# Kernel tuning notes

Measured on AMD Instinct MI355X. Metric: run time of the kernel, lower is better.

## Reference

```python
import jax, jax.numpy as jnp
import numpy as np

N_NODES = 100000

def _sage_layer(x, src, dst, W_self, W_neigh, b, act):
    # DGL SAGEConv 'mean': h = fc_self(x) + fc_neigh(mean_{u->v} x_u) + bias
    msg_sum = jax.ops.segment_sum(x[src], dst, num_segments=N_NODES)  # [N, d]
    deg = jax.ops.segment_sum(jnp.ones((src.shape[0], 1), x.dtype), dst, num_segments=N_NODES)
    h_neigh = msg_sum / jnp.maximum(deg, 1.0)
    h = x @ W_self + h_neigh @ W_neigh + b
    return jax.nn.relu(h) if act else h

def _edge_score(h, s, d, W1, b1, W2, b2):
    e = jnp.concatenate([h[s], h[d]], axis=-1)  # [E, 2*64]
    return (jax.nn.relu(e @ W1 + b1) @ W2 + b2).squeeze(-1)  # [E]

def setup_inputs() -> dict:
    key = jax.random.key(0)
    ks = jax.random.split(key, 16)
    E, EP = 1000000, 200000
    d_in, d_hid, d_out = 512, 256, 64
    def lin(k, fan_in, shape):
        return jax.random.normal(k, shape, dtype=jnp.float32) * (1.0 / np.sqrt(fan_in))
    return {
        "x": jax.random.normal(ks[0], (N_NODES, d_in), dtype=jnp.float32),
        "src": jax.random.randint(ks[1], (E,), 0, N_NODES, dtype=jnp.int32),
        "dst": jax.random.randint(ks[2], (E,), 0, N_NODES, dtype=jnp.int32),
        "pos_src": jax.random.randint(ks[3], (EP,), 0, N_NODES, dtype=jnp.int32),
        "pos_dst": jax.random.randint(ks[4], (EP,), 0, N_NODES, dtype=jnp.int32),
        "neg_src": jax.random.randint(ks[5], (EP,), 0, N_NODES, dtype=jnp.int32),
        "neg_dst": jax.random.randint(ks[6], (EP,), 0, N_NODES, dtype=jnp.int32),
        "W_self1": lin(ks[7], d_in, (d_in, d_hid)),
        "W_neigh1": lin(ks[8], d_in, (d_in, d_hid)),
        "b1": jnp.zeros((d_hid,), jnp.float32),
        "W_self2": lin(ks[9], d_hid, (d_hid, d_out)),
        "W_neigh2": lin(ks[10], d_hid, (d_hid, d_out)),
        "b2": jnp.zeros((d_out,), jnp.float32),
        "Wp1": lin(ks[11], 2 * d_out, (2 * d_out, d_out)),
        "bp1": jnp.zeros((d_out,), jnp.float32),
        "Wp2": lin(ks[12], d_out, (d_out, 1)),
        "bp2": jnp.zeros((1,), jnp.float32),
    }

def reference(x, src, dst, pos_src, pos_dst, neg_src, neg_dst,
              W_self1, W_neigh1, b1, W_self2, W_neigh2, b2,
              Wp1, bp1, Wp2, bp2):
    h = _sage_layer(x, src, dst, W_self1, W_neigh1, b1, act=True)
    h = _sage_layer(h, src, dst, W_self2, W_neigh2, b2, act=False)
    pos_score = _edge_score(h, pos_src, pos_dst, Wp1, bp1, Wp2, bp2)
    neg_score = _edge_score(h, neg_src, neg_dst, Wp1, bp1, Wp2, bp2)
    return (pos_score, neg_score)
```

## Files before the change

### kernel.cpp

```cpp
#include <hip/hip_runtime.h>
#include <hip/hip_bf16.h>


#define N_NODES 100000
#define N_EDGES 1000000
#define EPOS    200000
#define NSB     391

typedef unsigned short u16;
typedef unsigned int   u32;

typedef __bf16 bf16x8 __attribute__((ext_vector_type(8)));
typedef float  f32x4  __attribute__((ext_vector_type(4)));
typedef u16    u16x8  __attribute__((ext_vector_type(8)));

__device__ __forceinline__ u16 f2bf(float f) {
  u32 u = __float_as_uint(f);
  u32 r = (u + 0x7fffu + ((u >> 16) & 1u)) >> 16;
  return (u16)r;
}
__device__ __forceinline__ float bf2f(u16 h) {
  return __uint_as_float(((u32)h) << 16);
}

__device__ __forceinline__ void gl_lds16(const void* g, void* l) {
  __builtin_amdgcn_global_load_lds(
      (const __attribute__((address_space(1))) void*)g,
      (__attribute__((address_space(3))) void*)l, 16, 0, 0);
}

__global__ __launch_bounds__(256) void k_prep(
    const float* __restrict__ x, u16* __restrict__ xb,
    const int* __restrict__ dst, int* __restrict__ deg, int* __restrict__ epos,
    const float* __restrict__ Ws1, const float* __restrict__ Wn1, u16* __restrict__ W1t,
    const float* __restrict__ Ws2, const float* __restrict__ Wn2, u16* __restrict__ W2t,
    const float* __restrict__ Wp1, u16* __restrict__ Wpt) {
  const int bid = blockIdx.x;
  const int tid = threadIdx.x;
  if (bid < 25000) {
    long i = ((long)bid * 256 + tid) * 8;
    float4 f0 = *(const float4*)(x + i);
    float4 f1 = *(const float4*)(x + i + 4);
    u16x8 o;
    o[0] = f2bf(f0.x); o[1] = f2bf(f0.y); o[2] = f2bf(f0.z); o[3] = f2bf(f0.w);
    o[4] = f2bf(f1.x); o[5] = f2bf(f1.y); o[6] = f2bf(f1.z); o[7] = f2bf(f1.w);
    *(u16x8*)(xb + i) = o;
  } else if (bid < 28907) {
    int e = (bid - 25000) * 256 + tid;
    if (e < N_EDGES) epos[e] = atomicAdd(&deg[dst[e]], 1);
  } else if (bid < 29931) {
    int idx = (bid - 28907) * 256 + tid;
    int j = idx >> 9, k = idx & 511;
    float v = (j < 256) ? Ws1[k * 256 + j] : Wn1[k * 256 + (j - 256)];
    W1t[idx] = f2bf(v);
  } else if (bid < 30059) {
    int idx = (bid - 29931) * 256 + tid;
    int j = idx >> 8, k = idx & 255;
    float v = (j < 64) ? Ws2[k * 64 + j] : Wn2[k * 64 + (j - 64)];
    W2t[idx] = f2bf(v);
  } else {
    int idx = (bid - 30059) * 256 + tid;
    int j = idx >> 6, k = idx & 63;
    float v = (j < 64) ? Wp1[k * 64 + j] : Wp1[(64 + k) * 64 + (j - 64)];
    Wpt[idx] = f2bf(v);
  }
}

__global__ __launch_bounds__(256) void k_scan_a(const int* __restrict__ deg,
                                                int* __restrict__ bsum) {
  __shared__ int s[256];
  int i = blockIdx.x * 256 + threadIdx.x;
  s[threadIdx.x] = (i < N_NODES) ? deg[i] : 0;
  __syncthreads();
  for (int off = 128; off > 0; off >>= 1) {
    if (threadIdx.x < off) s[threadIdx.x] += s[threadIdx.x + off];
    __syncthreads();
  }
  if (threadIdx.x == 0) bsum[blockIdx.x] = s[0];
}

__global__ __launch_bounds__(512) void k_scan_b(int* __restrict__ bsum) {
  __shared__ int s[512];
  const int t = threadIdx.x;
  int v = (t < NSB) ? bsum[t] : 0;
  s[t] = v;
  __syncthreads();
  for (int off = 1; off < 512; off <<= 1) {
    int w = (t >= off) ? s[t - off] : 0;
    __syncthreads();
    s[t] += w;
    __syncthreads();
  }
  if (t < NSB) bsum[t] = s[t] - v;
}

__global__ __launch_bounds__(256) void k_scan_c(const int* __restrict__ deg,
                                                const int* __restrict__ bsum,
                                                int* __restrict__ offs,
                                                float* __restrict__ invdeg) {
  __shared__ int s[256];
  const int t = threadIdx.x;
  const int i = blockIdx.x * 256 + t;
  const int d = (i < N_NODES) ? deg[i] : 0;
  s[t] = d;
  __syncthreads();
  for (int off = 1; off < 256; off <<= 1) {
    int w = (t >= off) ? s[t - off] : 0;
    __syncthreads();
    s[t] += w;
    __syncthreads();
  }
  if (i < N_NODES) {
    const int base = bsum[blockIdx.x];
    offs[i] = base + s[t] - d;
    invdeg[i] = 1.0f / (float)(d > 0 ? d : 1);
    if (i == N_NODES - 1) offs[N_NODES] = base + s[t];
  }
}

__global__ void k_fill(const int* __restrict__ src, const int* __restrict__ dst,
                       const int* __restrict__ offs, const int* __restrict__ epos,
                       int* __restrict__ csr) {
  int i = blockIdx.x * 256 + threadIdx.x;
  if (i < N_EDGES) csr[offs[dst[i]] + epos[i]] = src[i];
}

template <bool OUT_F32, bool SWZ1>
__global__ __launch_bounds__(256) void gemm_bt(const u16* __restrict__ A,
                                               const u16* __restrict__ Bt,
                                               void* __restrict__ Cv,
                                               int M, int N, int K) {
  __shared__ u16 As[2][4096];
  __shared__ u16 Bs[2][4096];
  const int tid  = threadIdx.x;
  const int lane = tid & 63;
  const int wid  = tid >> 6;
  const int wr   = wid >> 1, wc = wid & 1;
  int bm0, bn0;
  if (SWZ1) {
    const int d = blockIdx.x;
    const int s = (d & 7) * 391 + (d >> 3);
    bm0 = (s >> 2) * 128;
    bn0 = (s & 3) * 128;
  } else {
    bm0 = blockIdx.y * 128;
    bn0 = blockIdx.x * 128;
  }

  const int sr = tid >> 2;
  const int sc = (tid & 3) * 8;
  const u16* pa0 = A  + (long)min(bm0 + sr,      M - 1) * K + sc;
  const u16* pa1 = A  + (long)min(bm0 + sr + 64, M - 1) * K + sc;
  const u16* pb0 = Bt + (long)(bn0 + sr)      * K + sc;
  const u16* pb1 = Bt + (long)(bn0 + sr + 64) * K + sc;
  const int lw = wid * 512;

  f32x4 acc[4][4];
#pragma unroll
  for (int i = 0; i < 4; ++i)
#pragma unroll
    for (int j = 0; j < 4; ++j) {
      f32x4 z = {0.f, 0.f, 0.f, 0.f};
      acc[i][j] = z;
    }

  const int nk = K >> 5;
#define STAGE(buf, kk) do { const int k0_ = (kk) << 5;                    \
    gl_lds16(pa0 + k0_, &As[buf][lw]);                                    \
    gl_lds16(pa1 + k0_, &As[buf][2048 + lw]);                             \
    gl_lds16(pb0 + k0_, &Bs[buf][lw]);                                    \
    gl_lds16(pb1 + k0_, &Bs[buf][2048 + lw]); } while (0)

  STAGE(0, 0);
  __syncthreads();
  int cur = 0;
  for (int kk = 0; kk < nk; ++kk) {
    if (kk + 1 < nk) STAGE(cur ^ 1, kk + 1);
    bf16x8 af[4], bfr[4];
#pragma unroll
    for (int mi = 0; mi < 4; ++mi)
      af[mi] = *reinterpret_cast<const bf16x8*>(
          &As[cur][(wr * 64 + mi * 16 + (lane & 15)) * 32 + ((lane >> 4) * 8)]);
#pragma unroll
    for (int ni = 0; ni < 4; ++ni)
      bfr[ni] = *reinterpret_cast<const bf16x8*>(
          &Bs[cur][(wc * 64 + ni * 16 + (lane & 15)) * 32 + ((lane >> 4) * 8)]);
#pragma unroll
    for (int mi = 0; mi < 4; ++mi)
#pragma unroll
      for (int ni = 0; ni < 4; ++ni)
        acc[mi][ni] = __builtin_amdgcn_mfma_f32_16x16x32_bf16(
            af[mi], bfr[ni], acc[mi][ni], 0, 0, 0);
    __syncthreads();
    cur ^= 1;
  }
#undef STAGE

  const int colb = bn0 + wc * 64 + (lane & 15);
  const int rowb = bm0 + wr * 64 + ((lane >> 4) * 4);
#pragma unroll
  for (int mi = 0; mi < 4; ++mi) {
#pragma unroll
    for (int ni = 0; ni < 4; ++ni) {
      const int col = colb + ni * 16;
#pragma unroll
      for (int e = 0; e < 4; ++e) {
        const int row = rowb + mi * 16 + e;
        if (row < M) {
          if (OUT_F32)
            ((float*)Cv)[(long)row * N + col] = acc[mi][ni][e];
          else
            ((u16*)Cv)[(long)row * N + col] = f2bf(acc[mi][ni][e]);
        }
      }
    }
  }
}

__global__ __launch_bounds__(256) void k_agg1(const u16* __restrict__ z1b,
                                              const int* __restrict__ csr,
                                              const int* __restrict__ offs,
                                              const float* __restrict__ invdeg,
                                              const float* __restrict__ b1,
                                              u16* __restrict__ h1b) {
  const int v    = blockIdx.x * 4 + (threadIdx.x >> 6);
  const int lane = threadIdx.x & 63;
  const int c    = lane * 4;
  const int o0 = offs[v], o1 = offs[v + 1];
  float a0 = 0.f, a1 = 0.f, a2 = 0.f, a3 = 0.f;
  int i = o0;
  for (; i + 8 <= o1; i += 8) {
    ushort4 q[8];
#pragma unroll
    for (int t = 0; t < 8; ++t)
      q[t] = *(const ushort4*)&z1b[(long)csr[i + t] * 512 + 256 + c];
#pragma unroll
    for (int t = 0; t < 8; ++t) {
      a0 += bf2f(q[t].x); a1 += bf2f(q[t].y);
      a2 += bf2f(q[t].z); a3 += bf2f(q[t].w);
    }
  }
  if (i + 4 <= o1) {
    ushort4 q[4];
#pragma unroll
    for (int t = 0; t < 4; ++t)
      q[t] = *(const ushort4*)&z1b[(long)csr[i + t] * 512 + 256 + c];
#pragma unroll
    for (int t = 0; t < 4; ++t) {
      a0 += bf2f(q[t].x); a1 += bf2f(q[t].y);
      a2 += bf2f(q[t].z); a3 += bf2f(q[t].w);
    }
    i += 4;
  }
  for (; i < o1; ++i) {
    ushort4 q = *(const ushort4*)&z1b[(long)csr[i] * 512 + 256 + c];
    a0 += bf2f(q.x); a1 += bf2f(q.y); a2 += bf2f(q.z); a3 += bf2f(q.w);
  }
  const float w = invdeg[v];
  ushort4 sf = *(const ushort4*)&z1b[(long)v * 512 + c];
  float4 bb = *(const float4*)&b1[c];
  ushort4 o;
  o.x = f2bf(fmaxf(bf2f(sf.x) + a0 * w + bb.x, 0.f));
  o.y = f2bf(fmaxf(bf2f(sf.y) + a1 * w + bb.y, 0.f));
  o.z = f2bf(fmaxf(bf2f(sf.z) + a2 * w + bb.z, 0.f));
  o.w = f2bf(fmaxf(bf2f(sf.w) + a3 * w + bb.w, 0.f));
  *(ushort4*)&h1b[(long)v * 256 + c] = o;
}

__global__ __launch_bounds__(256) void k_agg2(const u16* __restrict__ z2b,
                                              const int* __restrict__ csr,
                                              const int* __restrict__ offs,
                                              const float* __restrict__ invdeg,
                                              const float* __restrict__ b2,
                                              u16* __restrict__ h2b) {
  const int v    = blockIdx.x * 4 + (threadIdx.x >> 6);
  const int lane = threadIdx.x & 63;
  const int half = lane >> 5;
  const int c    = (lane & 31) * 2;
  const int o0 = offs[v], o1 = offs[v + 1];
  float a0 = 0.f, a1 = 0.f;
  int i = o0 + half;
  for (; i + 6 < o1; i += 8) {
    u32 q0 = *(const u32*)&z2b[(long)csr[i]     * 128 + 64 + c];
    u32 q1 = *(const u32*)&z2b[(long)csr[i + 2] * 128 + 64 + c];
    u32 q2 = *(const u32*)&z2b[(long)csr[i + 4] * 128 + 64 + c];
    u32 q3 = *(const u32*)&z2b[(long)csr[i + 6] * 128 + 64 + c];
    a0 += (bf2f((u16)q0) + bf2f((u16)q1)) + (bf2f((u16)q2) + bf2f((u16)q3));
    a1 += (bf2f((u16)(q0 >> 16)) + bf2f((u16)(q1 >> 16))) +
          (bf2f((u16)(q2 >> 16)) + bf2f((u16)(q3 >> 16)));
  }
  for (; i < o1; i += 2) {
    const u32 q = *(const u32*)&z2b[(long)csr[i] * 128 + 64 + c];
    a0 += bf2f((u16)q);
    a1 += bf2f((u16)(q >> 16));
  }
  a0 += __shfl_xor(a0, 32);
  a1 += __shfl_xor(a1, 32);
  if (half == 0) {
    const float w = invdeg[v];
    const u32 sq = *(const u32*)&z2b[(long)v * 128 + c];
    float h0 = bf2f((u16)sq) + a0 * w + b2[c];
    float h1 = bf2f((u16)(sq >> 16)) + a1 * w + b2[c + 1];
    u32 o = (u32)f2bf(h0) | ((u32)f2bf(h1) << 16);
    *(u32*)&h2b[(long)v * 64 + c] = o;
  }
}

__global__ __launch_bounds__(256) void k_edge(const u16* __restrict__ UVb,
                                              const int* __restrict__ ps,
                                              const int* __restrict__ pd,
                                              const int* __restrict__ ns,
                                              const int* __restrict__ nd,
                                              const float* __restrict__ bp1,
                                              const float* __restrict__ Wp2,
                                              const float* __restrict__ bp2,
                                              float* __restrict__ out) {
  const int g    = blockIdx.x * 4 + (threadIdx.x >> 6);
  const int lane = threadIdx.x & 63;
  const int half = lane >> 5;
  const int l    = lane & 31;
  int s, d;
  if (g < EPOS) { s = ps[g]; d = pd[g]; }
  else          { s = ns[g - EPOS]; d = nd[g - EPOS]; }
  const int node = half ? d : s;
  const u32 q = *(const u32*)&UVb[(long)node * 128 + half * 64 + 2 * l];
  float t0 = bf2f((u16)q), t1 = bf2f((u16)(q >> 16));
  t0 += __shfl_xor(t0, 32);
  t1 += __shfl_xor(t1, 32);
  const float2 bb = *(const float2*)&bp1[2 * l];
  const float2 ww = *(const float2*)&Wp2[2 * l];
  float p = fmaxf(t0 + bb.x, 0.f) * ww.x + fmaxf(t1 + bb.y, 0.f) * ww.y;
#pragma unroll
  for (int off = 16; off > 0; off >>= 1) p += __shfl_xor(p, off);
  if (lane == 0) out[g] = p + bp2[0];
}

extern "C" void kernel_launch(void* const* d_in, const int* in_sizes, int n_in,
                              void* d_out, int out_size, void* d_ws, size_t ws_size,
                              hipStream_t stream) {
  const float* x   = (const float*)d_in[0];
  const int*   src = (const int*)d_in[1];
  const int*   dst = (const int*)d_in[2];
  const int*   ps  = (const int*)d_in[3];
  const int*   pd  = (const int*)d_in[4];
  const int*   ns  = (const int*)d_in[5];
  const int*   nd  = (const int*)d_in[6];
  const float* Ws1 = (const float*)d_in[7];
  const float* Wn1 = (const float*)d_in[8];
  const float* b1  = (const float*)d_in[9];
  const float* Ws2 = (const float*)d_in[10];
  const float* Wn2 = (const float*)d_in[11];
  const float* b2  = (const float*)d_in[12];
  const float* Wp1 = (const float*)d_in[13];
  const float* bp1 = (const float*)d_in[14];
  const float* Wp2 = (const float*)d_in[15];
  const float* bp2 = (const float*)d_in[16];
  float* out = (float*)d_out;

  char* ws = (char*)d_ws;
  const size_t RB = 102400000;
  const size_t RC = 204800000;
  u16*   xb  = (u16*)(ws);
  u16*   h1b = (u16*)(ws);
  u16*   UVb = (u16*)(ws + 51200000);
  int*   epos= (int*)(ws + RB);
  u16*   z1b = (u16*)(ws + RB);
  u16*   z2b = (u16*)(ws + RB);
  u16*   h2b = (u16*)(ws + RB + 25600000);
  size_t o = RC;
  u16*   W1t = (u16*)(ws + o); o += 524288;
  u16*   W2t = (u16*)(ws + o); o += 65536;
  u16*   Wpt = (u16*)(ws + o); o += 16384;
  int*   deg = (int*)(ws + o); o += 400128;
  int*   offs= (int*)(ws + o); o += 400128;
  float* idg = (float*)(ws + o); o += 400128;
  int*   bsum= (int*)(ws + o); o += 2048;
  int*   csr = (int*)(ws + o); o += 4000000;
  (void)ws_size; (void)in_sizes; (void)n_in; (void)out_size;

  hipMemsetAsync(deg, 0, 400128, stream);

  k_prep<<<30091, 256, 0, stream>>>(x, xb, dst, deg, epos,
                                    Ws1, Wn1, W1t, Ws2, Wn2, W2t, Wp1, Wpt);
  k_scan_a<<<NSB, 256, 0, stream>>>(deg, bsum);
  k_scan_b<<<1, 512, 0, stream>>>(bsum);
  k_scan_c<<<NSB, 256, 0, stream>>>(deg, bsum, offs, idg);
  k_fill<<<3907, 256, 0, stream>>>(src, dst, offs, epos, csr);

  gemm_bt<false, true><<<3128, 256, 0, stream>>>(xb, W1t, z1b, N_NODES, 512, 512);
  k_agg1<<<25000, 256, 0, stream>>>(z1b, csr, offs, idg, b1, h1b);
  gemm_bt<false, false><<<dim3(1, 782), 256, 0, stream>>>(h1b, W2t, z2b, N_NODES, 128, 256);
  k_agg2<<<25000, 256, 0, stream>>>(z2b, csr, offs, idg, b2, h2b);
  gemm_bt<false, false><<<dim3(1, 782), 256, 0, stream>>>(h2b, Wpt, UVb, N_NODES, 128, 64);
  k_edge<<<100000, 256, 0, stream>>>(UVb, ps, pd, ns, nd, bp1, Wp2, bp2, out);
}
```

Baseline: 716.0 us.

## Fuse fp32-to-bf16 conversion of x into first GEMM and widen agg1 loads

Drops the separate pass that converted x to bf16 inside k_prep. The first GEMM now reads fp32 x directly, converts in registers, and writes to LDS, saving a 100 MB write and 100 MB re-read of xb. Because there are 4 column tiles, the first GEMM now reads the fp32 A rows from global memory once per column tile. Separately, k_agg1 now uses 16-byte loads with two half-waves splitting each node's edges and combining partial sums via a shuffle.

```diff
diff --git a/kernel.cpp b/kernel.cpp
--- a/kernel.cpp
+++ b/kernel.cpp
@@ -22,6 +22,12 @@
 __device__ __forceinline__ float bf2f(u16 h) {
   return __uint_as_float(((u32)h) << 16);
 }
+__device__ __forceinline__ u16x8 cvt8(float4 lo, float4 hi) {
+  u16x8 o;
+  o[0] = f2bf(lo.x); o[1] = f2bf(lo.y); o[2] = f2bf(lo.z); o[3] = f2bf(lo.w);
+  o[4] = f2bf(hi.x); o[5] = f2bf(hi.y); o[6] = f2bf(hi.z); o[7] = f2bf(hi.w);
+  return o;
+}
 
 __device__ __forceinline__ void gl_lds16(const void* g, void* l) {
   __builtin_amdgcn_global_load_lds(
@@ -30,36 +36,27 @@
 }
 
 __global__ __launch_bounds__(256) void k_prep(
-    const float* __restrict__ x, u16* __restrict__ xb,
     const int* __restrict__ dst, int* __restrict__ deg, int* __restrict__ epos,
     const float* __restrict__ Ws1, const float* __restrict__ Wn1, u16* __restrict__ W1t,
     const float* __restrict__ Ws2, const float* __restrict__ Wn2, u16* __restrict__ W2t,
     const float* __restrict__ Wp1, u16* __restrict__ Wpt) {
   const int bid = blockIdx.x;
   const int tid = threadIdx.x;
-  if (bid < 25000) {
-    long i = ((long)bid * 256 + tid) * 8;
-    float4 f0 = *(const float4*)(x + i);
-    float4 f1 = *(const float4*)(x + i + 4);
-    u16x8 o;
-    o[0] = f2bf(f0.x); o[1] = f2bf(f0.y); o[2] = f2bf(f0.z); o[3] = f2bf(f0.w);
-    o[4] = f2bf(f1.x); o[5] = f2bf(f1.y); o[6] = f2bf(f1.z); o[7] = f2bf(f1.w);
-    *(u16x8*)(xb + i) = o;
-  } else if (bid < 28907) {
-    int e = (bid - 25000) * 256 + tid;
+  if (bid < 3907) {
+    int e = bid * 256 + tid;
     if (e < N_EDGES) epos[e] = atomicAdd(&deg[dst[e]], 1);
-  } else if (bid < 29931) {
-    int idx = (bid - 28907) * 256 + tid;
+  } else if (bid < 4931) {
+    int idx = (bid - 3907) * 256 + tid;
     int j = idx >> 9, k = idx & 511;
     float v = (j < 256) ? Ws1[k * 256 + j] : Wn1[k * 256 + (j - 256)];
     W1t[idx] = f2bf(v);
-  } else if (bid < 30059) {
-    int idx = (bid - 29931) * 256 + tid;
+  } else if (bid < 5059) {
+    int idx = (bid - 4931) * 256 + tid;
     int j = idx >> 8, k = idx & 255;
     float v = (j < 64) ? Ws2[k * 64 + j] : Wn2[k * 64 + (j - 64)];
     W2t[idx] = f2bf(v);
   } else {
-    int idx = (bid - 30059) * 256 + tid;
+    int idx = (bid - 5059) * 256 + tid;
     int j = idx >> 6, k = idx & 63;
     float v = (j < 64) ? Wp1[k * 64 + j] : Wp1[(64 + k) * 64 + (j - 64)];
     Wpt[idx] = f2bf(v);
@@ -125,10 +122,96 @@
   if (i < N_EDGES) csr[offs[dst[i]] + epos[i]] = src[i];
 }
 
-template <bool OUT_F32, bool SWZ1>
+__global__ __launch_bounds__(256) void gemm1_f32(const float* __restrict__ A,
+                                                 const u16* __restrict__ Bt,
+                                                 u16* __restrict__ C, int M) {
+  const int K = 512, N = 512;
+  __shared__ u16 As[2][4096];
+  __shared__ u16 Bs[2][4096];
+  const int tid  = threadIdx.x;
+  const int lane = tid & 63;
+  const int wid  = tid >> 6;
+  const int wr   = wid >> 1, wc = wid & 1;
+  const int d    = blockIdx.x;
+  const int s    = (d & 7) * 391 + (d >> 3);
+  const int bm0  = (s >> 2) * 128;
+  const int bn0  = (s & 3) * 128;
+
+  const int sr = tid >> 2;
+  const int sc = (tid & 3) * 8;
+  const float* pa0 = A + (long)min(bm0 + sr,      M - 1) * K + sc;
+  const float* pa1 = A + (long)min(bm0 + sr + 64, M - 1) * K + sc;
+  const u16*   pb0 = Bt + (long)(bn0 + sr)      * K + sc;
+  const u16*   pb1 = Bt + (long)(bn0 + sr + 64) * K + sc;
+  const int lw = wid * 512;
+
+  f32x4 acc[4][4];
+#pragma unroll
+  for (int i = 0; i < 4; ++i)
+#pragma unroll
+    for (int j = 0; j < 4; ++j) {
+      f32x4 z = {0.f, 0.f, 0.f, 0.f};
+      acc[i][j] = z;
+    }
+
+  float4 r00, r01, r10, r11;
+#define LOADA(kk) do { const int k0_ = (kk) << 5;                         \
+    r00 = *(const float4*)(pa0 + k0_); r01 = *(const float4*)(pa0 + k0_ + 4); \
+    r10 = *(const float4*)(pa1 + k0_); r11 = *(const float4*)(pa1 + k0_ + 4); } while (0)
+#define STAGEB(buf, kk) do { const int k0_ = (kk) << 5;                   \
+    gl_lds16(pb0 + k0_, &Bs[buf][lw]);                                    \
+    gl_lds16(pb1 + k0_, &Bs[buf][2048 + lw]); } while (0)
+#define CVW(buf) do {                                                     \
+    *(u16x8*)&As[buf][sr * 32 + sc]        = cvt8(r00, r01);              \
+    *(u16x8*)&As[buf][(sr + 64) * 32 + sc] = cvt8(r10, r11); } while (0)
+
+  LOADA(0); STAGEB(0, 0); CVW(0);
+  __syncthreads();
+  int cur = 0;
+  const int nk = K >> 5;
+  for (int kk = 0; kk < nk; ++kk) {
+    if (kk + 1 < nk) { LOADA(kk + 1); STAGEB(cur ^ 1, kk + 1); }
+    bf16x8 af[4], bfr[4];
+#pragma unroll
+    for (int mi = 0; mi < 4; ++mi)
+      af[mi] = *reinterpret_cast<const bf16x8*>(
+          &As[cur][(wr * 64 + mi * 16 + (lane & 15)) * 32 + ((lane >> 4) * 8)]);
+#pragma unroll
+    for (int ni = 0; ni < 4; ++ni)
+      bfr[ni] = *reinterpret_cast<const bf16x8*>(
+          &Bs[cur][(wc * 64 + ni * 16 + (lane & 15)) * 32 + ((lane >> 4) * 8)]);
+#pragma unroll
+    for (int mi = 0; mi < 4; ++mi)
+#pragma unroll
+      for (int ni = 0; ni < 4; ++ni)
+        acc[mi][ni] = __builtin_amdgcn_mfma_f32_16x16x32_bf16(
+            af[mi], bfr[ni], acc[mi][ni], 0, 0, 0);
+    if (kk + 1 < nk) CVW(cur ^ 1);
+    __syncthreads();
+    cur ^= 1;
+  }
+#undef LOADA
+#undef STAGEB
+#undef CVW
+
+  const int colb = bn0 + wc * 64 + (lane & 15);
+  const int rowb = bm0 + wr * 64 + ((lane >> 4) * 4);
+#pragma unroll
+  for (int mi = 0; mi < 4; ++mi)
+#pragma unroll
+    for (int ni = 0; ni < 4; ++ni) {
+      const int col = colb + ni * 16;
+#pragma unroll
+      for (int e = 0; e < 4; ++e) {
+        const int row = rowb + mi * 16 + e;
+        if (row < M) C[(long)row * N + col] = f2bf(acc[mi][ni][e]);
+      }
+    }
+}
+
 __global__ __launch_bounds__(256) void gemm_bt(const u16* __restrict__ A,
                                                const u16* __restrict__ Bt,
-                                               void* __restrict__ Cv,
+                                               u16* __restrict__ C,
                                                int M, int N, int K) {
   __shared__ u16 As[2][4096];
   __shared__ u16 Bs[2][4096];
@@ -136,16 +219,8 @@
   const int lane = tid & 63;
   const int wid  = tid >> 6;
   const int wr   = wid >> 1, wc = wid & 1;
-  int bm0, bn0;
-  if (SWZ1) {
-    const int d = blockIdx.x;
-    const int s = (d & 7) * 391 + (d >> 3);
-    bm0 = (s >> 2) * 128;
-    bn0 = (s & 3) * 128;
-  } else {
-    bm0 = blockIdx.y * 128;
-    bn0 = blockIdx.x * 128;
-  }
+  const int bm0  = blockIdx.y * 128;
+  const int bn0  = blockIdx.x * 128;
 
   const int sr = tid >> 2;
   const int sc = (tid & 3) * 8;
@@ -199,22 +274,16 @@
   const int colb = bn0 + wc * 64 + (lane & 15);
   const int rowb = bm0 + wr * 64 + ((lane >> 4) * 4);
 #pragma unroll
-  for (int mi = 0; mi < 4; ++mi) {
+  for (int mi = 0; mi < 4; ++mi)
 #pragma unroll
     for (int ni = 0; ni < 4; ++ni) {
       const int col = colb + ni * 16;
 #pragma unroll
       for (int e = 0; e < 4; ++e) {
         const int row = rowb + mi * 16 + e;
-        if (row < M) {
-          if (OUT_F32)
-            ((float*)Cv)[(long)row * N + col] = acc[mi][ni][e];
-          else
-            ((u16*)Cv)[(long)row * N + col] = f2bf(acc[mi][ni][e]);
-        }
+        if (row < M) C[(long)row * N + col] = f2bf(acc[mi][ni][e]);
       }
     }
-  }
 }
 
 __global__ __launch_bounds__(256) void k_agg1(const u16* __restrict__ z1b,
@@ -225,46 +294,41 @@
                                               u16* __restrict__ h1b) {
   const int v    = blockIdx.x * 4 + (threadIdx.x >> 6);
   const int lane = threadIdx.x & 63;
-  const int c    = lane * 4;
+  const int half = lane >> 5;
+  const int c    = (lane & 31) * 8;
   const int o0 = offs[v], o1 = offs[v + 1];
-  float a0 = 0.f, a1 = 0.f, a2 = 0.f, a3 = 0.f;
-  int i = o0;
-  for (; i + 8 <= o1; i += 8) {
-    ushort4 q[8];
-#pragma unroll
-    for (int t = 0; t < 8; ++t)
-      q[t] = *(const ushort4*)&z1b[(long)csr[i + t] * 512 + 256 + c];
-#pragma unroll
-    for (int t = 0; t < 8; ++t) {
-      a0 += bf2f(q[t].x); a1 += bf2f(q[t].y);
-      a2 += bf2f(q[t].z); a3 += bf2f(q[t].w);
-    }
-  }
-  if (i + 4 <= o1) {
-    ushort4 q[4];
-#pragma unroll
-    for (int t = 0; t < 4; ++t)
-      q[t] = *(const ushort4*)&z1b[(long)csr[i + t] * 512 + 256 + c];
-#pragma unroll
-    for (int t = 0; t < 4; ++t) {
-      a0 += bf2f(q[t].x); a1 += bf2f(q[t].y);
-      a2 += bf2f(q[t].z); a3 += bf2f(q[t].w);
-    }
-    i += 4;
-  }
-  for (; i < o1; ++i) {
-    ushort4 q = *(const ushort4*)&z1b[(long)csr[i] * 512 + 256 + c];
-    a0 += bf2f(q.x); a1 += bf2f(q.y); a2 += bf2f(q.z); a3 += bf2f(q.w);
-  }
-  const float w = invdeg[v];
-  ushort4 sf = *(const ushort4*)&z1b[(long)v * 512 + c];
-  float4 bb = *(const float4*)&b1[c];
-  ushort4 o;
-  o.x = f2bf(fmaxf(bf2f(sf.x) + a0 * w + bb.x, 0.f));
-  o.y = f2bf(fmaxf(bf2f(sf.y) + a1 * w + bb.y, 0.f));
-  o.z = f2bf(fmaxf(bf2f(sf.z) + a2 * w + bb.z, 0.f));
-  o.w = f2bf(fmaxf(bf2f(sf.w) + a3 * w + bb.w, 0.f));
-  *(ushort4*)&h1b[(long)v * 256 + c] = o;
+  float a[8];
+#pragma unroll
+  for (int e = 0; e < 8; ++e) a[e] = 0.f;
+  int i = o0 + half;
+  for (; i + 6 < o1; i += 8) {
+    u16x8 q0 = *(const u16x8*)&z1b[(long)csr[i]     * 512 + 256 + c];
+    u16x8 q1 = *(const u16x8*)&z1b[(long)csr[i + 2] * 512 + 256 + c];
+    u16x8 q2 = *(const u16x8*)&z1b[(long)csr[i + 4] * 512 + 256 + c];
+    u16x8 q3 = *(const u16x8*)&z1b[(long)csr[i + 6] * 512 + 256 + c];
+#pragma unroll
+    for (int e = 0; e < 8; ++e)
+      a[e] += (bf2f(q0[e]) + bf2f(q1[e])) + (bf2f(q2[e]) + bf2f(q3[e]));
+  }
+  for (; i < o1; i += 2) {
+    u16x8 q = *(const u16x8*)&z1b[(long)csr[i] * 512 + 256 + c];
+#pragma unroll
+    for (int e = 0; e < 8; ++e) a[e] += bf2f(q[e]);
+  }
+#pragma unroll
+  for (int e = 0; e < 8; ++e) a[e] += __shfl_xor(a[e], 32);
+  if (half == 0) {
+    const float w = invdeg[v];
+    u16x8 sf = *(const u16x8*)&z1b[(long)v * 512 + c];
+    float4 bb0 = *(const float4*)&b1[c];
+    float4 bb1 = *(const float4*)&b1[c + 4];
+    float bb[8] = {bb0.x, bb0.y, bb0.z, bb0.w, bb1.x, bb1.y, bb1.z, bb1.w};
+    u16x8 o;
+#pragma unroll
+    for (int e = 0; e < 8; ++e)
+      o[e] = f2bf(fmaxf(bf2f(sf[e]) + a[e] * w + bb[e], 0.f));
+    *(u16x8*)&h1b[(long)v * 256 + c] = o;
+  }
 }
 
 __global__ __launch_bounds__(256) void k_agg2(const u16* __restrict__ z2b,
@@ -360,7 +424,6 @@
   char* ws = (char*)d_ws;
   const size_t RB = 102400000;
   const size_t RC = 204800000;
-  u16*   xb  = (u16*)(ws);
   u16*   h1b = (u16*)(ws);
   u16*   UVb = (u16*)(ws + 51200000);
   int*   epos= (int*)(ws + RB);
@@ -380,17 +443,17 @@
 
   hipMemsetAsync(deg, 0, 400128, stream);
 
-  k_prep<<<30091, 256, 0, stream>>>(x, xb, dst, deg, epos,
-                                    Ws1, Wn1, W1t, Ws2, Wn2, W2t, Wp1, Wpt);
+  k_prep<<<5091, 256, 0, stream>>>(dst, deg, epos,
+                                   Ws1, Wn1, W1t, Ws2, Wn2, W2t, Wp1, Wpt);
   k_scan_a<<<NSB, 256, 0, stream>>>(deg, bsum);
   k_scan_b<<<1, 512, 0, stream>>>(bsum);
   k_scan_c<<<NSB, 256, 0, stream>>>(deg, bsum, offs, idg);
   k_fill<<<3907, 256, 0, stream>>>(src, dst, offs, epos, csr);
 
-  gemm_bt<false, true><<<3128, 256, 0, stream>>>(xb, W1t, z1b, N_NODES, 512, 512);
+  gemm1_f32<<<3128, 256, 0, stream>>>(x, W1t, z1b, N_NODES);
   k_agg1<<<25000, 256, 0, stream>>>(z1b, csr, offs, idg, b1, h1b);
-  gemm_bt<false, false><<<dim3(1, 782), 256, 0, stream>>>(h1b, W2t, z2b, N_NODES, 128, 256);
+  gemm_bt<<<dim3(1, 782), 256, 0, stream>>>(h1b, W2t, z2b, N_NODES, 128, 256);
   k_agg2<<<25000, 256, 0, stream>>>(z2b, csr, offs, idg, b2, h2b);
-  gemm_bt<false, false><<<dim3(1, 782), 256, 0, stream>>>(h2b, Wpt, UVb, N_NODES, 128, 64);
+  gemm_bt<<<dim3(1, 782), 256, 0, stream>>>(h2b, Wpt, UVb, N_NODES, 128, 64);
   k_edge<<<100000, 256, 0, stream>>>(UVb, ps, pd, ns, nd, bp1, Wp2, bp2, out);
 }
```

After: 705.9 us. About the same (-1.4%).
